# Optimization experiments

Measured on AMD Instinct MI355X. Metric: run time of the kernel, lower is better.

The kernel has to match this reference:

```python
import jax, jax.numpy as jnp
import numpy as np

E = 4       # num_edge_types
DEPTH = 3   # args.depth (weight_tying=False -> DEPTH message layers)
V = 117     # num_atom_types


def setup_inputs() -> dict:
    key = jax.random.key(0)
    ks = jax.random.split(key, 13)
    mb, atoms, D, M = 1024, 128, 256, 512
    s = 0.05  # weight scale
    return {
        "atom_array": jax.random.randint(ks[0], (mb, atoms), 0, V),
        "adj": jax.random.uniform(ks[1], (mb, E, atoms, atoms), dtype=jnp.float32),
        "embed": jax.random.normal(ks[2], (V, D), jnp.float32) * s,
        "msg_W": jax.random.normal(ks[3], (DEPTH, E * D, D), jnp.float32) * s,
        "msg_b": jnp.zeros((DEPTH, E * D), jnp.float32),
        "W_ih": jax.random.normal(ks[4], (3 * D, D), jnp.float32) * s,
        "b_ih": jnp.zeros((3 * D,), jnp.float32),
        "W_hh": jax.random.normal(ks[5], (3 * D, D), jnp.float32) * s,
        "b_hh": jnp.zeros((3 * D,), jnp.float32),
        "i_W": jax.random.normal(ks[6], (M, 2 * D), jnp.float32) * s,
        "i_b": jnp.zeros((M,), jnp.float32),
        "j_W": jax.random.normal(ks[7], (M, D), jnp.float32) * s,
        "j_b": jnp.zeros((M,), jnp.float32),
    }


def _gru_cell(x, h, W_ih, b_ih, W_hh, b_hh):
    # PyTorch GRUCell math. x: input (message), h: hidden state.
    gi = x @ W_ih.T + b_ih
    gh = h @ W_hh.T + b_hh
    ir, iz, in_ = jnp.split(gi, 3, axis=-1)
    hr, hz, hn = jnp.split(gh, 3, axis=-1)
    r = jax.nn.sigmoid(ir + hr)
    z = jax.nn.sigmoid(iz + hz)
    n = jnp.tanh(in_ + r * hn)
    return (1.0 - z) * n + z * h


def reference(atom_array, adj, embed, msg_W, msg_b, W_ih, b_ih, W_hh, b_hh, i_W, i_b, j_W, j_b):
    mb, atoms = atom_array.shape
    D = embed.shape[1]
    h = embed[atom_array]          # [mb, atoms, D]
    h0 = h
    for step in range(DEPTH):
        # message: Linear(D -> E*D) then per-edge-type adjacency bmm, summed over edge types
        m = h @ msg_W[step].T + msg_b[step]            # [mb, atoms, E*D]
        m = m.reshape(mb, atoms, E, D).transpose(0, 2, 1, 3)  # [mb, E, atoms, D]
        m = jnp.einsum('beij,bejd->bid', adj, m)       # bmm + sum over edge types
        hid = h if step > 0 else jnp.zeros_like(h)     # GRUCell(hidden=None) at step 0
        h = _gru_cell(m, hid, W_ih, b_ih, W_hh, b_hh)  # [mb, atoms, D]
    # gated readout
    gate = jax.nn.sigmoid(jnp.concatenate([h, h0], axis=-1) @ i_W.T + i_b)  # [mb, atoms, M]
    val = h @ j_W.T + j_b                                                    # [mb, atoms, M]
    return jnp.sum(gate * val, axis=1)                                       # [mb, M]
```

## Files before the change

### kernel.cpp

```cpp
#include <hip/hip_runtime.h>
#include <cstdint>
#include <cstddef>

using f32x4 = float __attribute__((ext_vector_type(4)));
using u16x8 = unsigned short __attribute__((ext_vector_type(8)));
using u16x4 = unsigned short __attribute__((ext_vector_type(4)));
typedef _Float16 f16x8 __attribute__((ext_vector_type(8)));

#define DEV static __device__ __forceinline__

DEV unsigned short f2h(float f) {
  _Float16 x = (_Float16)f;
  return __builtin_bit_cast(unsigned short, x);
}
DEV float h2f(unsigned short s) {
  return (float)__builtin_bit_cast(_Float16, s);
}
DEV float sigm(float x) { return 1.f / (1.f + __expf(-x)); }
DEV float tanh_(float x) { return 2.f / (1.f + __expf(-2.f * x)) - 1.f; }

#define MFMA_F16(acc, va, vb) \
  acc = __builtin_amdgcn_mfma_f32_16x16x32_f16(va, vb, acc, 0, 0, 0)

constexpr int NB = 1024;
constexpr int AT = 128;
constexpr int DD = 256;
constexpr int MOUT = 512;
constexpr long NR = (long)NB * AT;

#define VWAIT(n) do { asm volatile("s_waitcnt vmcnt(" #n ")" ::: "memory"); \
                      __builtin_amdgcn_sched_barrier(0); } while (0)
#define BARR do { __builtin_amdgcn_sched_barrier(0); __builtin_amdgcn_s_barrier(); \
                  __builtin_amdgcn_sched_barrier(0); } while (0)

__global__ __launch_bounds__(256) void k_cvt(const float* __restrict__ src,
                                             unsigned short* __restrict__ dst) {
  long base = ((long)blockIdx.x * 256 + threadIdx.x) * 8;
  f32x4 v0 = *(const f32x4*)(src + base);
  f32x4 v1 = *(const f32x4*)(src + base + 4);
  u16x8 o;
  #pragma unroll
  for (int q = 0; q < 4; ++q) o[q] = f2h(v0[q]);
  #pragma unroll
  for (int q = 0; q < 4; ++q) o[4 + q] = f2h(v1[q]);
  *(u16x8*)(dst + base) = o;
}

__global__ __launch_bounds__(256) void k_cvt5(const float* __restrict__ s0, unsigned short* __restrict__ d0,
                                              const float* __restrict__ s1, unsigned short* __restrict__ d1,
                                              const float* __restrict__ s2, unsigned short* __restrict__ d2,
                                              const float* __restrict__ s3, unsigned short* __restrict__ d3,
                                              const float* __restrict__ s4, unsigned short* __restrict__ d4) {
  int blk = blockIdx.x;
  const float* s; unsigned short* d;
  if (blk < 384)      { s = s0; d = d0; }
  else if (blk < 480) { s = s1; d = d1; blk -= 384; }
  else if (blk < 576) { s = s2; d = d2; blk -= 480; }
  else if (blk < 704) { s = s3; d = d3; blk -= 576; }
  else                { s = s4; d = d4; blk -= 704; }
  long base = ((long)blk * 256 + threadIdx.x) * 8;
  f32x4 v0 = *(const f32x4*)(s + base);
  f32x4 v1 = *(const f32x4*)(s + base + 4);
  u16x8 o;
  #pragma unroll
  for (int q = 0; q < 4; ++q) o[q] = f2h(v0[q]);
  #pragma unroll
  for (int q = 0; q < 4; ++q) o[4 + q] = f2h(v1[q]);
  *(u16x8*)(d + base) = o;
}

__global__ __launch_bounds__(256) void k_gather(const int* __restrict__ atom,
                                                const float* __restrict__ embed,
                                                unsigned short* __restrict__ h,
                                                unsigned short* __restrict__ h0) {
  long idx = (long)blockIdx.x * 256 + threadIdx.x;
  long n = idx >> 6;
  int ch = (int)(idx & 63);
  int a = atom[n];
  f32x4 v = *(const f32x4*)(embed + (size_t)a * DD + ch * 4);
  u16x4 o;
  #pragma unroll
  for (int q = 0; q < 4; ++q) o[q] = f2h(v[q]);
  *(u16x4*)(h  + n * DD + ch * 4) = o;
  *(u16x4*)(h0 + n * DD + ch * 4) = o;
}

#define GEMM_IDS \
  const int tid = threadIdx.x, lane = tid & 63, wave = tid >> 6; \
  const int wr = wave >> 1, wc = wave & 1; \
  const int l15 = lane & 15, lg = lane >> 4; \
  const int sseg = (l15 >> 1) & 3;

#define GLDS(SRC, STRIDE, DST) \
  { \
    _Pragma("unroll") \
    for (int j_ = 0; j_ < 2; ++j_) { \
      const unsigned short* g_ = (SRC) + \
          (size_t)((wave * 2 + j_) * 16 + (lane >> 2)) * (STRIDE) + \
          ((lane & 3) ^ ((lane >> 3) & 3)) * 8; \
      __builtin_amdgcn_global_load_lds( \
          (const __attribute__((address_space(1))) void*)g_, \
          (__attribute__((address_space(3))) void*)&DST[(wave * 2 + j_) * 16][0], \
          16, 0, 0); \
    } \
  }

#define GLDS64(SRC, STRIDE, DST) \
  { \
    const unsigned short* g_ = (SRC) + \
        (size_t)(wave * 16 + (lane >> 2)) * (STRIDE) + \
        ((lane & 3) ^ ((lane >> 3) & 3)) * 8; \
    __builtin_amdgcn_global_load_lds( \
        (const __attribute__((address_space(1))) void*)g_, \
        (__attribute__((address_space(3))) void*)&DST[wave * 16][0], \
        16, 0, 0); \
  }

#define LOAD_A(AH) \
  f16x8 ah[4]; \
  _Pragma("unroll") \
  for (int m_ = 0; m_ < 4; ++m_) \
    ah[m_] = *(const f16x8*)&AH[wr * 64 + m_ * 16 + l15][(lg ^ sseg) * 8];

#define LOAD_B(BH) \
  f16x8 bh[4]; \
  _Pragma("unroll") \
  for (int n_ = 0; n_ < 4; ++n_) \
    bh[n_] = *(const f16x8*)&BH[wc * 64 + n_ * 16 + l15][(lg ^ sseg) * 8];

#define MFMA_TILE(ACC) \
  _Pragma("unroll") \
  for (int m_ = 0; m_ < 4; ++m_) \
    _Pragma("unroll") \
    for (int n_ = 0; n_ < 4; ++n_) \
      MFMA_F16(ACC[m_][n_], ah[m_], bh[n_]);

__global__ __launch_bounds__(256) void k_msgadj(const unsigned short* __restrict__ h,
                                                const unsigned short* __restrict__ W,
                                                const float* __restrict__ bias,
                                                const unsigned short* __restrict__ adjh,
                                                unsigned short* __restrict__ m_out) {
  __shared__ unsigned short As[128][32], Bs[128][32];
  __shared__ unsigned short PT[128][136];
  GEMM_IDS
  const size_t b = blockIdx.x;
  const int d0 = blockIdx.y * 128;
  f32x4 accM[4][4] = {};
  for (int e = 0; e < 4; ++e) {
    f32x4 accP[4][4] = {};
    for (int k0 = 0; k0 < 256; k0 += 32) {
      GLDS(h + (b * 128) * 256 + k0, 256, As)
      GLDS(W + (size_t)(e * 256 + d0) * 256 + k0, 256, Bs)
      __syncthreads();
      LOAD_A(As)
      LOAD_B(Bs)
      MFMA_TILE(accP)
      __syncthreads();
    }
    #pragma unroll
    for (int m_ = 0; m_ < 4; ++m_) {
      int j0 = wr * 64 + m_ * 16 + lg * 4;
      #pragma unroll
      for (int n_ = 0; n_ < 4; ++n_) {
        int c = wc * 64 + n_ * 16 + l15;
        float bb = bias[e * 256 + d0 + c];
        u16x4 o;
        #pragma unroll
        for (int q = 0; q < 4; ++q) o[q] = f2h(accP[m_][n_][q] + bb);
        *(u16x4*)&PT[c][j0] = o;
      }
    }
    __syncthreads();
    for (int kt = 0; kt < 4; ++kt) {
      const int jk = kt * 32;
      GLDS(adjh + (((size_t)b * 4 + e) * 128) * 128 + jk, 128, As)
      __syncthreads();
      LOAD_A(As)
      f16x8 bh[4];
      #pragma unroll
      for (int n_ = 0; n_ < 4; ++n_)
        bh[n_] = *(const f16x8*)&PT[wc * 64 + n_ * 16 + l15][jk + lg * 8];
      MFMA_TILE(accM)
      __syncthreads();
    }
  }
  #pragma unroll
  for (int m_ = 0; m_ < 4; ++m_) {
    int i0 = wr * 64 + m_ * 16 + lg * 4;
    #pragma unroll
    for (int n_ = 0; n_ < 4; ++n_) {
      int c = d0 + wc * 64 + n_ * 16 + l15;
      #pragma unroll
      for (int q = 0; q < 4; ++q)
        m_out[((size_t)b * 128 + i0 + q) * 256 + c] = f2h(accM[m_][n_][q]);
    }
  }
}

template <bool HAS_H>
__global__ __launch_bounds__(256) void k_grufuse(const unsigned short* __restrict__ m,
                                                 const unsigned short* __restrict__ h,
                                                 const unsigned short* __restrict__ wih,
                                                 const unsigned short* __restrict__ whh,
                                                 const float* __restrict__ b_ih,
                                                 const float* __restrict__ b_hh,
                                                 unsigned short* __restrict__ h_new) {
  __shared__ unsigned short As[3][64][32];
  __shared__ unsigned short Br[3][64][32], Bz[3][64][32], Bn[3][64][32];
  GEMM_IDS
  const size_t b = blockIdx.x;
  const int quad = blockIdx.y;
  const int r0 = (quad >> 2) * 64;
  const int c0 = (quad & 3) * 64;
  const unsigned short* msrc = m + ((size_t)b * 128 + r0) * 256;
  const unsigned short* hsrc = h + ((size_t)b * 128 + r0) * 256;
  constexpr int NKT = HAS_H ? 16 : 8;

  f32x4 accR[2][2] = {}, accZ[2][2] = {}, accI[2][2] = {}, accN[2][2] = {};

  auto stage = [&](int t, int s) {
    const unsigned short* a_ = ((HAS_H && t >= 8) ? hsrc : msrc) + (t & 7) * 32;
    const unsigned short* w_ = (HAS_H && t >= 8) ? whh : wih;
    GLDS64(a_, 256, As[s])
    GLDS64(w_ + (size_t)(c0) * 256 + (t & 7) * 32, 256, Br[s])
    GLDS64(w_ + (size_t)(256 + c0) * 256 + (t & 7) * 32, 256, Bz[s])
    GLDS64(w_ + (size_t)(512 + c0) * 256 + (t & 7) * 32, 256, Bn[s])
  };

  stage(0, 0);
  stage(1, 1);
  #pragma unroll
  for (int kt = 0; kt < NKT; ++kt) {
    const int cur = kt % 3;
    if (kt + 2 < NKT) stage(kt + 2, (kt + 2) % 3);
    if (kt + 2 < NKT) { VWAIT(8); } else if (kt + 2 == NKT) { VWAIT(4); } else { VWAIT(0); }
    BARR;
    f16x8 af[2], brf[2], bzf[2], bnf[2];
    #pragma unroll
    for (int m_ = 0; m_ < 2; ++m_)
      af[m_] = *(const f16x8*)&As[cur][wr * 32 + m_ * 16 + l15][(lg ^ sseg) * 8];
    #pragma unroll
    for (int n_ = 0; n_ < 2; ++n_) {
      brf[n_] = *(const f16x8*)&Br[cur][wc * 32 + n_ * 16 + l15][(lg ^ sseg) * 8];
      bzf[n_] = *(const f16x8*)&Bz[cur][wc * 32 + n_ * 16 + l15][(lg ^ sseg) * 8];
      bnf[n_] = *(const f16x8*)&Bn[cur][wc * 32 + n_ * 16 + l15][(lg ^ sseg) * 8];
    }
    #pragma unroll
    for (int m_ = 0; m_ < 2; ++m_)
      #pragma unroll
      for (int n_ = 0; n_ < 2; ++n_) {
        MFMA_F16(accR[m_][n_], af[m_], brf[n_]);
        MFMA_F16(accZ[m_][n_], af[m_], bzf[n_]);
        if (!HAS_H || kt < 8) { MFMA_F16(accI[m_][n_], af[m_], bnf[n_]); }
        else                  { MFMA_F16(accN[m_][n_], af[m_], bnf[n_]); }
      }
    BARR;
  }

  #pragma unroll
  for (int m_ = 0; m_ < 2; ++m_) {
    int rloc = r0 + wr * 32 + m_ * 16 + lg * 4;
    #pragma unroll
    for (int n_ = 0; n_ < 2; ++n_) {
      int c = c0 + wc * 32 + n_ * 16 + l15;
      float br = b_ih[c] + b_hh[c];
      float bz = b_ih[256 + c] + b_hh[256 + c];
      float bin = b_ih[512 + c], bhn = b_hh[512 + c];
      #pragma unroll
      for (int q = 0; q < 4; ++q) {
        size_t row = (size_t)b * 128 + rloc + q;
        float r = sigm(accR[m_][n_][q] + br);
        float z = sigm(accZ[m_][n_][q] + bz);
        float hn = (HAS_H ? accN[m_][n_][q] : 0.f) + bhn;
        float nn = tanh_(accI[m_][n_][q] + bin + r * hn);
        float hv = HAS_H ? h2f(h[row * 256 + c]) : 0.f;
        h_new[row * 256 + c] = f2h((1.f - z) * nn + z * hv);
      }
    }
  }
}

__global__ __launch_bounds__(256) void k_readout(const unsigned short* __restrict__ h,
                                                 const unsigned short* __restrict__ h0,
                                                 const unsigned short* __restrict__ iw,
                                                 const unsigned short* __restrict__ jw,
                                                 const float* __restrict__ ib,
                                                 const float* __restrict__ jb,
                                                 float* __restrict__ out) {
  __shared__ unsigned short As[2][128][32];
  __shared__ unsigned short Bg[2][128][32], Bv[2][128][32];
  __shared__ float red[2][128];
  GEMM_IDS
  const size_t b = blockIdx.x;
  const int c0 = blockIdx.y * 128;
  auto as_src = [&](int t) {
    return (t < 8) ? (h + b * 128 * 256 + t * 32) : (h0 + b * 128 * 256 + (t - 8) * 32);
  };
  f32x4 accG[4][4] = {};
  f32x4 accV[4][4] = {};
  GLDS(as_src(0), 256, As[0])
  GLDS(iw + (size_t)c0 * 512, 512, Bg[0])
  GLDS(jw + (size_t)c0 * 256, 256, Bv[0])
  #pragma unroll
  for (int kt = 0; kt < 16; ++kt) {
    const int cur = kt & 1;
    if (kt + 1 < 16) {
      GLDS(as_src(kt + 1), 256, As[cur ^ 1])
      GLDS(iw + (size_t)c0 * 512 + (kt + 1) * 32, 512, Bg[cur ^ 1])
      if (kt + 1 < 8) GLDS(jw + (size_t)c0 * 256 + (kt + 1) * 32, 256, Bv[cur ^ 1])
    }
    if (kt < 7) { VWAIT(6); } else if (kt < 15) { VWAIT(4); } else { VWAIT(0); }
    BARR;
    LOAD_A(As[cur])
    f16x8 bg[4];
    #pragma unroll
    for (int n_ = 0; n_ < 4; ++n_)
      bg[n_] = *(const f16x8*)&Bg[cur][wc * 64 + n_ * 16 + l15][(lg ^ sseg) * 8];
    #pragma unroll
    for (int m_ = 0; m_ < 4; ++m_)
      #pragma unroll
      for (int n_ = 0; n_ < 4; ++n_)
        MFMA_F16(accG[m_][n_], ah[m_], bg[n_]);
    if (kt < 8) {
      f16x8 bv[4];
      #pragma unroll
      for (int n_ = 0; n_ < 4; ++n_)
        bv[n_] = *(const f16x8*)&Bv[cur][wc * 64 + n_ * 16 + l15][(lg ^ sseg) * 8];
      #pragma unroll
      for (int m_ = 0; m_ < 4; ++m_)
        #pragma unroll
        for (int n_ = 0; n_ < 4; ++n_)
          MFMA_F16(accV[m_][n_], ah[m_], bv[n_]);
    }
    BARR;
  }
  #pragma unroll
  for (int n_ = 0; n_ < 4; ++n_) {
    int c = c0 + wc * 64 + n_ * 16 + l15;
    float gb = ib[c], vb = jb[c];
    float s = 0.f;
    #pragma unroll
    for (int m_ = 0; m_ < 4; ++m_)
      #pragma unroll
      for (int q = 0; q < 4; ++q) {
        float g = sigm(accG[m_][n_][q] + gb);
        float v = accV[m_][n_][q] + vb;
        s += g * v;
      }
    s += __shfl_xor(s, 16);
    s += __shfl_xor(s, 32);
    if (lg == 0) red[wr][wc * 64 + n_ * 16 + l15] = s;
  }
  __syncthreads();
  if (tid < 128) out[b * MOUT + c0 + tid] = red[0][tid] + red[1][tid];
}

extern "C" void kernel_launch(void* const* d_in, const int* in_sizes, int n_in,
                              void* d_out, int out_size, void* d_ws, size_t ws_size,
                              hipStream_t stream) {
  const int*   atom  = (const int*)d_in[0];
  const float* adj   = (const float*)d_in[1];
  const float* embed = (const float*)d_in[2];
  const float* msg_W = (const float*)d_in[3];
  const float* msg_b = (const float*)d_in[4];
  const float* W_ih  = (const float*)d_in[5];
  const float* b_ih  = (const float*)d_in[6];
  const float* W_hh  = (const float*)d_in[7];
  const float* b_hh  = (const float*)d_in[8];
  const float* i_W   = (const float*)d_in[9];
  const float* i_b   = (const float*)d_in[10];
  const float* j_W   = (const float*)d_in[11];
  const float* j_b   = (const float*)d_in[12];
  float* out = (float*)d_out;

  const size_t SZ_H   = (size_t)NR * 256 * 2;
  const size_t SZ_ADJ = (size_t)NB * 4 * 128 * 128 * 2;

  char* p = (char*)d_ws;
  unsigned short* hA   = (unsigned short*)p;  p += SZ_H;
  unsigned short* hB   = (unsigned short*)p;  p += SZ_H;
  unsigned short* h0   = (unsigned short*)p;  p += SZ_H;
  unsigned short* m    = (unsigned short*)p;  p += SZ_H;
  unsigned short* adjh = (unsigned short*)p;  p += SZ_ADJ;
  unsigned short* wmsg = (unsigned short*)p;  p += (size_t)3 * 1024 * 256 * 2;
  unsigned short* wih  = (unsigned short*)p;  p += (size_t)768 * 256 * 2;
  unsigned short* whh  = (unsigned short*)p;  p += (size_t)768 * 256 * 2;
  unsigned short* wiw  = (unsigned short*)p;  p += (size_t)512 * 512 * 2;
  unsigned short* wjw  = (unsigned short*)p;  p += (size_t)512 * 256 * 2;
  if ((size_t)(p - (char*)d_ws) > ws_size) return;

  k_cvt<<<(int)((size_t)NB * 4 * 128 * 128 / 2048), 256, 0, stream>>>(adj, adjh);
  k_cvt5<<<768, 256, 0, stream>>>(msg_W, wmsg, W_ih, wih, W_hh, whh, i_W, wiw, j_W, wjw);

  k_gather<<<(int)(NR * 64 / 256), 256, 0, stream>>>(atom, embed, hA, h0);

  unsigned short* h_cur = hA;
  unsigned short* h_nxt = hB;
  for (int step = 0; step < 3; ++step) {
    k_msgadj<<<dim3(NB, 2), 256, 0, stream>>>(h_cur, wmsg + (size_t)step * 262144,
                                              msg_b + (size_t)step * 1024, adjh, m);
    if (step == 0)
      k_grufuse<false><<<dim3(NB, 8), 256, 0, stream>>>(m, h_cur, wih, whh, b_ih, b_hh, h_nxt);
    else
      k_grufuse<true><<<dim3(NB, 8), 256, 0, stream>>>(m, h_cur, wih, whh, b_ih, b_hh, h_nxt);
    unsigned short* t = h_cur; h_cur = h_nxt; h_nxt = t;
  }

  k_readout<<<dim3(NB, 4), 256, 0, stream>>>(h_cur, h0, wiw, wjw, i_b, j_b, out);
}
```

Before: 1.220 ms.

## Double-buffer msg/adj GEMM loads and shrink GRU pipeline to two stages

After: 1.219 ms. Within noise of the previous version (-0.1%).

```diff
diff --git a/kernel.cpp b/kernel.cpp
--- a/kernel.cpp
+++ b/kernel.cpp
@@ -30,6 +30,8 @@
 
 #define VWAIT(n) do { asm volatile("s_waitcnt vmcnt(" #n ")" ::: "memory"); \
                       __builtin_amdgcn_sched_barrier(0); } while (0)
+#define LWAIT do { asm volatile("s_waitcnt lgkmcnt(0)" ::: "memory"); \
+                   __builtin_amdgcn_sched_barrier(0); } while (0)
 #define BARR do { __builtin_amdgcn_sched_barrier(0); __builtin_amdgcn_s_barrier(); \
                   __builtin_amdgcn_sched_barrier(0); } while (0)
 
@@ -140,22 +142,45 @@
                                                 const float* __restrict__ bias,
                                                 const unsigned short* __restrict__ adjh,
                                                 unsigned short* __restrict__ m_out) {
-  __shared__ unsigned short As[128][32], Bs[128][32];
-  __shared__ unsigned short PT[128][136];
+  __shared__ __align__(16) char pool[16384 + 128 * 136 * 2];
+  typedef unsigned short row32[32];
+  row32* As_[2] = { (row32*)pool,          (row32*)(pool + 16384) };
+  row32* Bs_[2] = { (row32*)(pool + 8192), (row32*)(pool + 24576) };
+  unsigned short (*PT)[136] = (unsigned short (*)[136])(pool + 16384);
   GEMM_IDS
   const size_t b = blockIdx.x;
   const int d0 = blockIdx.y * 128;
+  const unsigned short* hb = h + (size_t)b * 128 * 256;
+  const unsigned short* adjb = adjh + (size_t)b * 4 * 128 * 128;
   f32x4 accM[4][4] = {};
   for (int e = 0; e < 4; ++e) {
     f32x4 accP[4][4] = {};
-    for (int k0 = 0; k0 < 256; k0 += 32) {
-      GLDS(h + (b * 128) * 256 + k0, 256, As)
-      GLDS(W + (size_t)(e * 256 + d0) * 256 + k0, 256, Bs)
-      __syncthreads();
-      LOAD_A(As)
-      LOAD_B(Bs)
-      MFMA_TILE(accP)
-      __syncthreads();
+    const unsigned short* We = W + (size_t)(e * 256 + d0) * 256;
+    const unsigned short* adje = adjb + (size_t)e * 128 * 128;
+    GLDS(hb, 256, As_[0])
+    GLDS(We, 256, Bs_[0])
+    #pragma unroll
+    for (int k0i = 0; k0i < 8; ++k0i) {
+      const int cur = k0i & 1;
+      if (k0i < 7) {
+        row32* an_ = As_[cur ^ 1];
+        row32* bn_ = Bs_[cur ^ 1];
+        GLDS(hb + (k0i + 1) * 32, 256, an_)
+        GLDS(We + (k0i + 1) * 32, 256, bn_)
+      } else {
+        GLDS(adje + 0 * 32, 128, As_[0])
+        GLDS(adje + 1 * 32, 128, Bs_[0])
+      }
+      VWAIT(4);
+      BARR;
+      {
+        row32* ac_ = As_[cur];
+        row32* bc_ = Bs_[cur];
+        LOAD_A(ac_)
+        LOAD_B(bc_)
+        MFMA_TILE(accP)
+      }
+      BARR;
     }
     #pragma unroll
     for (int m_ = 0; m_ < 4; ++m_) {
@@ -170,18 +195,24 @@
         *(u16x4*)&PT[c][j0] = o;
       }
     }
-    __syncthreads();
+    LWAIT;
+    BARR;
+    #pragma unroll
     for (int kt = 0; kt < 4; ++kt) {
-      const int jk = kt * 32;
-      GLDS(adjh + (((size_t)b * 4 + e) * 128) * 128 + jk, 128, As)
-      __syncthreads();
-      LOAD_A(As)
-      f16x8 bh[4];
-      #pragma unroll
-      for (int n_ = 0; n_ < 4; ++n_)
-        bh[n_] = *(const f16x8*)&PT[wc * 64 + n_ * 16 + l15][jk + lg * 8];
-      MFMA_TILE(accM)
-      __syncthreads();
+      if (kt == 1) { GLDS(adje + 2 * 32, 128, As_[0]) }
+      if (kt == 2) { GLDS(adje + 3 * 32, 128, Bs_[0]) }
+      if (kt < 3) { VWAIT(2); } else { VWAIT(0); }
+      BARR;
+      {
+        row32* ac_ = (kt & 1) ? Bs_[0] : As_[0];
+        LOAD_A(ac_)
+        f16x8 bh[4];
+        #pragma unroll
+        for (int n_ = 0; n_ < 4; ++n_)
+          bh[n_] = *(const f16x8*)&PT[wc * 64 + n_ * 16 + l15][kt * 32 + lg * 8];
+        MFMA_TILE(accM)
+      }
+      BARR;
     }
   }
   #pragma unroll
@@ -205,8 +236,8 @@
                                                  const float* __restrict__ b_ih,
                                                  const float* __restrict__ b_hh,
                                                  unsigned short* __restrict__ h_new) {
-  __shared__ unsigned short As[3][64][32];
-  __shared__ unsigned short Br[3][64][32], Bz[3][64][32], Bn[3][64][32];
+  __shared__ unsigned short As[2][64][32];
+  __shared__ unsigned short Br[2][64][32], Bz[2][64][32], Bn[2][64][32];
   GEMM_IDS
   const size_t b = blockIdx.x;
   const int quad = blockIdx.y;
@@ -228,12 +259,11 @@
   };
 
   stage(0, 0);
-  stage(1, 1);
   #pragma unroll
   for (int kt = 0; kt < NKT; ++kt) {
-    const int cur = kt % 3;
-    if (kt + 2 < NKT) stage(kt + 2, (kt + 2) % 3);
-    if (kt + 2 < NKT) { VWAIT(8); } else if (kt + 2 == NKT) { VWAIT(4); } else { VWAIT(0); }
+    const int cur = kt & 1;
+    if (kt + 1 < NKT) stage(kt + 1, cur ^ 1);
+    if (kt + 1 < NKT) { VWAIT(4); } else { VWAIT(0); }
     BARR;
     f16x8 af[2], brf[2], bzf[2], bnf[2];
     #pragma unroll
```
